# Performance work log

Hardware: AMD Instinct MI355X
Metric: run time of the kernel (lower is better)

Reference implementation:

```python
import jax, jax.numpy as jnp
import numpy as np

DIM_MODEL = 1024
NHEAD = 16
DIM_HEAD = DIM_MODEL // NHEAD


def setup_inputs() -> dict:
    key = jax.random.key(0)
    k1, k2, k3, k4 = jax.random.split(key, 4)
    x = jax.random.normal(k1, (4, 2048, DIM_MODEL), dtype=jnp.float32)
    # nn.Linear weights: PyTorch stores [out, in]; we keep [in, out] for x @ W.
    s = 1.0 / np.sqrt(DIM_MODEL)
    w_qkv = jax.random.uniform(k2, (DIM_MODEL, 3 * DIM_MODEL), jnp.float32, -s, s)
    w_out = jax.random.uniform(k3, (DIM_MODEL, DIM_MODEL), jnp.float32, -s, s)
    b_out = jax.random.uniform(k4, (DIM_MODEL,), jnp.float32, -s, s)
    return {"x": x, "w_qkv": w_qkv, "w_out": w_out, "b_out": b_out}


def reference(x, w_qkv, w_out, b_out):
    b, n, _ = x.shape
    scale = DIM_HEAD ** -0.5
    qkv = x @ w_qkv                              # [b, n, 3*dim]
    q, k, v = jnp.split(qkv, 3, axis=-1)
    def split_heads(t):                          # [b, n, h*d] -> [b, h, n, d]
        return t.reshape(b, n, NHEAD, DIM_HEAD).transpose(0, 2, 1, 3)
    q, k, v = split_heads(q), split_heads(k), split_heads(v)
    attn = jnp.einsum('bhnd,bhmd->bhnm', q, k) * scale
    attn = jax.nn.softmax(attn, axis=-1)
    out = jnp.einsum('bhnm,bhmd->bhnd', attn, v)
    out = out.transpose(0, 2, 1, 3).reshape(b, n, NHEAD * DIM_HEAD)
    return out @ w_out + b_out
```

## Files before the change

### kernel.cpp

```cpp
#include <hip/hip_runtime.h>
#include <math.h>

#define DM   1024
#define NH   16
#define DH   64
#define SEQ  2048
#define BATCH 4
#define QSCALE 0.18033688011112042f

typedef __attribute__((ext_vector_type(8)))  short short8;
typedef __attribute__((ext_vector_type(4)))  float f32x4;
typedef __attribute__((ext_vector_type(16))) float f32x16;

static __device__ __forceinline__ unsigned short f2bf(float f) {
    unsigned u = __float_as_uint(f);
    unsigned r = (u + 0x7fffu + ((u >> 16) & 1u)) >> 16;
    return (unsigned short)r;
}

#define GLD(gp, lp) __builtin_amdgcn_global_load_lds( \
    (const __attribute__((address_space(1))) void*)(gp), \
    (__attribute__((address_space(3))) void*)(lp), 16, 0, 0)

__global__ __launch_bounds__(256) void prep_all(
    const float* __restrict__ x, unsigned short* __restrict__ x_h,
    const float* __restrict__ w_qkv, unsigned short* __restrict__ wqT_h,
    const float* __restrict__ w_out, unsigned short* __restrict__ woT_h)
{
    __shared__ float t[32][33];
    const int bid = blockIdx.x;
    const int tid = threadIdx.x;
    if (bid < 8192) {
        int i = bid * 256 + tid;
        float4 v = reinterpret_cast<const float4*>(x)[i];
        ushort4 h;
        h.x = f2bf(v.x); h.y = f2bf(v.y); h.z = f2bf(v.z); h.w = f2bf(v.w);
        reinterpret_cast<ushort4*>(x_h)[i] = h;
        return;
    }
    const float* in;
    unsigned short* outT;
    int K = DM, N, n0, k0;
    if (bid < 8192 + 3072) {
        int bb = bid - 8192;
        in = w_qkv; outT = wqT_h; N = 3 * DM;
        n0 = (bb % 96) * 32; k0 = (bb / 96) * 32;
    } else {
        int bb = bid - 8192 - 3072;
        in = w_out; outT = woT_h; N = DM;
        n0 = (bb % 32) * 32; k0 = (bb / 32) * 32;
    }
    const int tx = tid & 31, ty = tid >> 5;
    #pragma unroll
    for (int r = 0; r < 32; r += 8)
        t[ty + r][tx] = in[(size_t)(k0 + ty + r) * N + n0 + tx];
    __syncthreads();
    #pragma unroll
    for (int r = 0; r < 32; r += 8)
        outT[(size_t)(n0 + ty + r) * K + k0 + tx] = f2bf(t[tx][ty + r]);
}

__global__ __launch_bounds__(256) void gemm_qkv(
    const unsigned short* __restrict__ Ah, const unsigned short* __restrict__ Bh,
    unsigned short* __restrict__ Qh, unsigned short* __restrict__ Kph,
    unsigned short* __restrict__ Vph, int M, int N, int K)
{
    __shared__ __align__(16) unsigned short sAh[128 * 32];
    __shared__ __align__(16) unsigned short sBh[128 * 32];

    const int tid = threadIdx.x;
    const int l = tid & 63, w = tid >> 6;
    const int wr = w >> 1, wc = w & 1;

    int nwg = gridDim.x * gridDim.y;
    int lin = blockIdx.x + gridDim.x * blockIdx.y;
    int cpx = nwg >> 3;
    int nl = (lin & 7) * cpx + (lin >> 3);
    const int bm = (nl % gridDim.x) * 128, bn = (nl / gridDim.x) * 128;

    const int srow = w * 32 + (l >> 2);
    const int scol = (l & 3) * 8;
    const size_t a0 = (size_t)(bm + srow) * K + scol;
    const size_t a1 = (size_t)(bm + srow + 16) * K + scol;
    const size_t b0 = (size_t)(bn + srow) * K + scol;
    const size_t b1 = (size_t)(bn + srow + 16) * K + scol;

    const int fr = l & 15;
    const int fk = (l >> 4) * 8;

    f32x4 acc[4][4];
    #pragma unroll
    for (int i = 0; i < 4; ++i)
        #pragma unroll
        for (int j = 0; j < 4; ++j)
            acc[i][j] = (f32x4){0.f, 0.f, 0.f, 0.f};

    for (int k0 = 0; k0 < K; k0 += 32) {
        __syncthreads();
        GLD(Ah + a0 + k0, sAh + w * 1024);
        GLD(Ah + a1 + k0, sAh + w * 1024 + 512);
        GLD(Bh + b0 + k0, sBh + w * 1024);
        GLD(Bh + b1 + k0, sBh + w * 1024 + 512);
        __syncthreads();

        short8 vah[4], vbh[4];
        #pragma unroll
        for (int i = 0; i < 4; ++i) {
            int ar = (wr * 64 + i * 16 + fr) * 32 + fk;
            int br = (wc * 64 + i * 16 + fr) * 32 + fk;
            vah[i] = *reinterpret_cast<const short8*>(&sAh[ar]);
            vbh[i] = *reinterpret_cast<const short8*>(&sBh[br]);
        }
        __builtin_amdgcn_s_setprio(1);
        #pragma unroll
        for (int i = 0; i < 4; ++i)
            #pragma unroll
            for (int j = 0; j < 4; ++j)
                acc[i][j] = __builtin_amdgcn_mfma_f32_16x16x32_bf16(vah[i], vbh[j], acc[i][j], 0, 0, 0);
        __builtin_amdgcn_s_setprio(0);
    }

    #pragma unroll
    for (int i = 0; i < 4; ++i) {
        #pragma unroll
        for (int j = 0; j < 4; ++j) {
            int row0 = bm + wr * 64 + i * 16 + (l >> 4) * 4;
            int col  = bn + wc * 64 + j * 16 + fr;
            if (col < 1024) {
                #pragma unroll
                for (int r = 0; r < 4; ++r)
                    Qh[(size_t)(row0 + r) * 1024 + col] = f2bf(acc[i][j][r] * QSCALE);
            } else if (col < 2048) {
                int sec = col - 1024, head = sec >> 6, d = sec & 63;
                int pK = ((d >> 4) << 1) | ((d >> 3) & 1);
                int d7 = d & 7;
                #pragma unroll
                for (int r = 0; r < 4; ++r) {
                    int row = row0 + r;
                    int bb = row >> 11, seq = row & 2047;
                    int kt = seq >> 6, k64 = seq & 63;
                    int p = ((k64 >> 5) << 3) + pK;
                    size_t addr = ((((size_t)(bb * 16 + head) * 32 + kt) * 512)
                                   + p * 32 + (k64 & 31)) * 8 + d7;
                    Kph[addr] = f2bf(acc[i][j][r]);
                }
            } else {
                int sec = col - 2048, head = sec >> 6, d = sec & 63;
                int row = row0;
                int bb = row >> 11, seq = row & 2047;
                int kt = seq >> 6, k64 = seq & 63, k16 = k64 & 15;
                int p = ((d >> 5) << 3) + ((k64 >> 4) << 1) + ((k16 >> 2) & 1);
                int jbase = (k16 >> 3) << 2;
                size_t chunk = (((size_t)(bb * 16 + head) * 32 + kt) * 512
                                + p * 32 + (d & 31));
                ushort4 v4;
                #pragma unroll
                for (int r = 0; r < 4; ++r)
                    ((unsigned short*)&v4)[r] = f2bf(acc[i][j][r]);
                *reinterpret_cast<ushort4*>(Vph + chunk * 8 + jbase) = v4;
            }
        }
    }
}

__global__ __launch_bounds__(256) void gemm_out(
    const unsigned short* __restrict__ Ah, const unsigned short* __restrict__ Bh,
    const float* __restrict__ bias, float* __restrict__ C, int M, int N, int K)
{
    __shared__ __align__(16) unsigned short sAh[128 * 32];
    __shared__ __align__(16) unsigned short sBh[128 * 32];

    const int tid = threadIdx.x;
    const int l = tid & 63, w = tid >> 6;
    const int wr = w >> 1, wc = w & 1;

    int nwg = gridDim.x * gridDim.y;
    int lin = blockIdx.x + gridDim.x * blockIdx.y;
    int cpx = nwg >> 3;
    int nl = (lin & 7) * cpx + (lin >> 3);
    const int bm = (nl % gridDim.x) * 128, bn = (nl / gridDim.x) * 128;

    const int srow = w * 32 + (l >> 2);
    const int scol = (l & 3) * 8;
    const size_t a0 = (size_t)(bm + srow) * K + scol;
    const size_t a1 = (size_t)(bm + srow + 16) * K + scol;
    const size_t b0 = (size_t)(bn + srow) * K + scol;
    const size_t b1 = (size_t)(bn + srow + 16) * K + scol;

    const int fr = l & 15;
    const int fk = (l >> 4) * 8;

    f32x4 acc[4][4];
    #pragma unroll
    for (int i = 0; i < 4; ++i)
        #pragma unroll
        for (int j = 0; j < 4; ++j)
            acc[i][j] = (f32x4){0.f, 0.f, 0.f, 0.f};

    for (int k0 = 0; k0 < K; k0 += 32) {
        __syncthreads();
        GLD(Ah + a0 + k0, sAh + w * 1024);
        GLD(Ah + a1 + k0, sAh + w * 1024 + 512);
        GLD(Bh + b0 + k0, sBh + w * 1024);
        GLD(Bh + b1 + k0, sBh + w * 1024 + 512);
        __syncthreads();

        short8 vah[4], vbh[4];
        #pragma unroll
        for (int i = 0; i < 4; ++i) {
            int ar = (wr * 64 + i * 16 + fr) * 32 + fk;
            int br = (wc * 64 + i * 16 + fr) * 32 + fk;
            vah[i] = *reinterpret_cast<const short8*>(&sAh[ar]);
            vbh[i] = *reinterpret_cast<const short8*>(&sBh[br]);
        }
        __builtin_amdgcn_s_setprio(1);
        #pragma unroll
        for (int i = 0; i < 4; ++i)
            #pragma unroll
            for (int j = 0; j < 4; ++j)
                acc[i][j] = __builtin_amdgcn_mfma_f32_16x16x32_bf16(vah[i], vbh[j], acc[i][j], 0, 0, 0);
        __builtin_amdgcn_s_setprio(0);
    }

    #pragma unroll
    for (int i = 0; i < 4; ++i) {
        #pragma unroll
        for (int j = 0; j < 4; ++j) {
            int row = bm + wr * 64 + i * 16 + (l >> 4) * 4;
            int col = bn + wc * 64 + j * 16 + fr;
            float bb = bias[col];
            #pragma unroll
            for (int r = 0; r < 4; ++r)
                C[(size_t)(row + r) * N + col] = acc[i][j][r] + bb;
        }
    }
}

__global__ __launch_bounds__(256, 3) void flash_attn_mfma(
    const unsigned short* __restrict__ Qh,
    const unsigned short* __restrict__ Kph,
    const unsigned short* __restrict__ Vph,
    unsigned short* __restrict__ out_hi)
{
    __shared__ __align__(16) unsigned short sK[2][4096];
    __shared__ __align__(16) unsigned short sV[2][4096];

    int lin = blockIdx.x + 16 * blockIdx.y + 256 * blockIdx.z;
    int nlid = (lin & 7) * 128 + (lin >> 3);
    const int qt = nlid & 15, head = (nlid >> 4) & 15, b = nlid >> 8;

    const int tid = threadIdx.x;
    const int l = tid & 63, w = tid >> 6;
    const int q5 = l & 31, hf = l >> 5;

    const int bh = b * NH + head;
    const size_t kvb = (size_t)bh * 32 * 512 * 8;

    #define STAGE_KV(cbuf, kt_) do {                                          \
        _Pragma("unroll")                                                     \
        for (int i2 = 0; i2 < 2; ++i2) {                                      \
            int ch = (w * 2 + i2) * 64 + l;                                   \
            size_t s8 = kvb + ((size_t)(kt_) * 512 + ch) * 8;                 \
            GLD(Kph + s8, (char*)&sK[cbuf][0] + ch * 16);                     \
            GLD(Vph + s8, (char*)&sV[cbuf][0] + ch * 16);                     \
        }                                                                     \
    } while (0)

    const int qrow = qt * 128 + w * 32 + q5;
    short8 qhr[4];
    {
        const size_t qb = ((size_t)b * SEQ + qrow) * 1024 + head * 64;
        #pragma unroll
        for (int s = 0; s < 4; ++s)
            qhr[s] = *reinterpret_cast<const short8*>(Qh + qb + s * 16 + hf * 8);
    }

    float l_ = 0.f;
    f32x16 oacc0, oacc1, fz;
    #pragma unroll
    for (int r = 0; r < 16; ++r) { oacc0[r] = 0.f; oacc1[r] = 0.f; fz[r] = 0.f; }

    union FragU { unsigned u[4]; short8 s8; };
    short8 pbh[4];

    STAGE_KV(0, 0);
    int cur = 0;

    for (int kt = 0; kt < SEQ / 64; ++kt) {
        __syncthreads();
        if (kt + 1 < SEQ / 64) STAGE_KV(cur ^ 1, kt + 1);

        const char* kb = (const char*)&sK[cur][0] + l * 16;

        f32x16 sacc0, sacc1;
        __builtin_amdgcn_s_setprio(1);
        {
            short8 k0h = *reinterpret_cast<const short8*>(kb);
            short8 k1h = *reinterpret_cast<const short8*>(kb + 4 * 1024);
            sacc0 = __builtin_amdgcn_mfma_f32_32x32x16_bf16(k0h, qhr[0], fz, 0, 0, 0);
            sacc1 = __builtin_amdgcn_mfma_f32_32x32x16_bf16(k1h, qhr[0], fz, 0, 0, 0);
        }
        #pragma unroll
        for (int s = 1; s < 4; ++s) {
            short8 k0h = *reinterpret_cast<const short8*>(kb + s * 1024);
            short8 k1h = *reinterpret_cast<const short8*>(kb + (4 + s) * 1024);
            sacc0 = __builtin_amdgcn_mfma_f32_32x32x16_bf16(k0h, qhr[s], sacc0, 0, 0, 0);
            sacc1 = __builtin_amdgcn_mfma_f32_32x32x16_bf16(k1h, qhr[s], sacc1, 0, 0, 0);
        }
        __builtin_amdgcn_s_setprio(0);

        float ssum = 0.f;
        #pragma unroll
        for (int jt = 0; jt < 2; ++jt) {
            float pv[16];
            #pragma unroll
            for (int r = 0; r < 16; ++r) {
                float sv = (jt == 0) ? sacc0[r] : sacc1[r];
                pv[r] = __builtin_amdgcn_exp2f(sv);
                ssum += pv[r];
            }
            FragU f0, f1;
            asm("v_cvt_pk_bf16_f32 %0, %1, %2" : "=v"(f0.u[0]) : "v"(pv[0]),  "v"(pv[1]));
            asm("v_cvt_pk_bf16_f32 %0, %1, %2" : "=v"(f0.u[1]) : "v"(pv[2]),  "v"(pv[3]));
            asm("v_cvt_pk_bf16_f32 %0, %1, %2" : "=v"(f0.u[2]) : "v"(pv[4]),  "v"(pv[5]));
            asm("v_cvt_pk_bf16_f32 %0, %1, %2" : "=v"(f0.u[3]) : "v"(pv[6]),  "v"(pv[7]));
            asm("v_cvt_pk_bf16_f32 %0, %1, %2" : "=v"(f1.u[0]) : "v"(pv[8]),  "v"(pv[9]));
            asm("v_cvt_pk_bf16_f32 %0, %1, %2" : "=v"(f1.u[1]) : "v"(pv[10]), "v"(pv[11]));
            asm("v_cvt_pk_bf16_f32 %0, %1, %2" : "=v"(f1.u[2]) : "v"(pv[12]), "v"(pv[13]));
            asm("v_cvt_pk_bf16_f32 %0, %1, %2" : "=v"(f1.u[3]) : "v"(pv[14]), "v"(pv[15]));
            pbh[jt * 2 + 0] = f0.s8;
            pbh[jt * 2 + 1] = f1.s8;
        }
        l_ += ssum;

        const char* vb = (const char*)&sV[cur][0] + l * 16;
        __builtin_amdgcn_s_setprio(1);
        #pragma unroll
        for (int kpv = 0; kpv < 4; ++kpv) {
            short8 v0h = *reinterpret_cast<const short8*>(vb + kpv * 1024);
            short8 v1h = *reinterpret_cast<const short8*>(vb + (4 + kpv) * 1024);
            oacc0 = __builtin_amdgcn_mfma_f32_32x32x16_bf16(v0h, pbh[kpv], oacc0, 0, 0, 0);
            oacc1 = __builtin_amdgcn_mfma_f32_32x32x16_bf16(v1h, pbh[kpv], oacc1, 0, 0, 0);
        }
        __builtin_amdgcn_s_setprio(0);
        cur ^= 1;
    }

    l_ += __shfl_xor(l_, 32);
    float linv = 1.f / l_;
    #pragma unroll
    for (int dt = 0; dt < 2; ++dt) {
        #pragma unroll
        for (int rq = 0; rq < 4; ++rq) {
            int dbase = dt * 32 + rq * 8 + 4 * hf;
            ushort4 h4;
            #pragma unroll
            for (int c = 0; c < 4; ++c) {
                float v = ((dt == 0) ? oacc0[rq * 4 + c] : oacc1[rq * 4 + c]) * linv;
                ((unsigned short*)&h4)[c] = f2bf(v);
            }
            size_t o = ((size_t)b * SEQ + qrow) * DM + head * 64 + dbase;
            *reinterpret_cast<ushort4*>(out_hi + o) = h4;
        }
    }
    #undef STAGE_KV
}

extern "C" void kernel_launch(void* const* d_in, const int* in_sizes, int n_in,
                              void* d_out, int out_size, void* d_ws, size_t ws_size,
                              hipStream_t stream) {
    const float* x     = (const float*)d_in[0];
    const float* w_qkv = (const float*)d_in[1];
    const float* w_out = (const float*)d_in[2];
    const float* b_out = (const float*)d_in[3];
    float* out = (float*)d_out;

    const int M = BATCH * SEQ;

    char* ws = (char*)d_ws;
    unsigned short* x_h   = (unsigned short*)ws;                         ws += (size_t)M * DM * 2;
    unsigned short* Qh    = (unsigned short*)ws;                         ws += (size_t)M * DM * 2;
    unsigned short* Kp_h  = (unsigned short*)ws;                         ws += (size_t)M * DM * 2;
    unsigned short* Vp_h  = (unsigned short*)ws;                         ws += (size_t)M * DM * 2;
    unsigned short* wqT_h = (unsigned short*)ws;                         ws += (size_t)3072 * DM * 2;
    unsigned short* woT_h = (unsigned short*)ws;                         ws += (size_t)DM * DM * 2;
    unsigned short* at_hi = (unsigned short*)ws;

    dim3 blk(256);

    prep_all<<<dim3(8192 + 3072 + 1024), blk, 0, stream>>>(
        x, x_h, w_qkv, wqT_h, w_out, woT_h);

    gemm_qkv<<<dim3(M / 128, 3 * DM / 128), blk, 0, stream>>>(
        x_h, wqT_h, Qh, Kp_h, Vp_h, M, 3 * DM, DM);

    flash_attn_mfma<<<dim3(SEQ / 128, NH, BATCH), blk, 0, stream>>>(
        Qh, Kp_h, Vp_h, at_hi);

    gemm_out<<<dim3(M / 128, DM / 128), blk, 0, stream>>>(
        at_hi, woT_h, b_out, out, M, DM, DM);
}
```

Baseline: 196.9 us.

## Pre-pack GEMM operands into MFMA fragment-tiled layout for contiguous LDS loads

The prep kernel now writes x and both weight matrices as bf16 in a tile-packed layout of 128x32 blocks, ordered so that each GEMM k-step is one contiguous 8 KB chunk. The attention kernel writes its output in the same packed layout. Both GEMMs then issue fully contiguous global-to-LDS loads and read fragments with lane-linear LDS addresses, which removes strided row access and likely LDS bank conflicts. The trade-off is that the transposing weight pack now uses strided scalar reads without an LDS transpose, and the GEMMs are hard-coded to fixed shapes.

```diff
diff --git a/kernel.cpp b/kernel.cpp
--- a/kernel.cpp
+++ b/kernel.cpp
@@ -3,7 +3,6 @@
 
 #define DM   1024
 #define NH   16
-#define DH   64
 #define SEQ  2048
 #define BATCH 4
 #define QSCALE 0.18033688011112042f
@@ -22,51 +21,52 @@
     (const __attribute__((address_space(1))) void*)(gp), \
     (__attribute__((address_space(3))) void*)(lp), 16, 0, 0)
 
-__global__ __launch_bounds__(256) void prep_all(
-    const float* __restrict__ x, unsigned short* __restrict__ x_h,
-    const float* __restrict__ w_qkv, unsigned short* __restrict__ wqT_h,
-    const float* __restrict__ w_out, unsigned short* __restrict__ woT_h)
+__global__ __launch_bounds__(256) void prep_pack(
+    const float* __restrict__ x,     unsigned short* __restrict__ xp,
+    const float* __restrict__ wq,    unsigned short* __restrict__ wqp,
+    const float* __restrict__ wo,    unsigned short* __restrict__ wop)
 {
-    __shared__ float t[32][33];
-    const int bid = blockIdx.x;
-    const int tid = threadIdx.x;
-    if (bid < 8192) {
-        int i = bid * 256 + tid;
-        float4 v = reinterpret_cast<const float4*>(x)[i];
-        ushort4 h;
-        h.x = f2bf(v.x); h.y = f2bf(v.y); h.z = f2bf(v.z); h.w = f2bf(v.w);
-        reinterpret_cast<ushort4*>(x_h)[i] = h;
-        return;
-    }
-    const float* in;
-    unsigned short* outT;
-    int K = DM, N, n0, k0;
-    if (bid < 8192 + 3072) {
-        int bb = bid - 8192;
-        in = w_qkv; outT = wqT_h; N = 3 * DM;
-        n0 = (bb % 96) * 32; k0 = (bb / 96) * 32;
-    } else {
-        int bb = bid - 8192 - 3072;
-        in = w_out; outT = woT_h; N = DM;
-        n0 = (bb % 32) * 32; k0 = (bb / 32) * 32;
-    }
-    const int tx = tid & 31, ty = tid >> 5;
-    #pragma unroll
-    for (int r = 0; r < 32; r += 8)
-        t[ty + r][tx] = in[(size_t)(k0 + ty + r) * N + n0 + tx];
-    __syncthreads();
-    #pragma unroll
-    for (int r = 0; r < 32; r += 8)
-        outT[(size_t)(n0 + ty + r) * K + k0 + tx] = f2bf(t[tx][ty + r]);
+    const int bid = blockIdx.x, t = threadIdx.x;
+    const float* src; unsigned short* dst; int C, tile_n, tile_k; bool trans;
+    if (bid < 2048)      { src = x;  dst = xp;  C = 1024; trans = false;
+                           tile_n = bid >> 5;          tile_k = bid & 31; }
+    else if (bid < 2816) { int bb = bid - 2048; src = wq; dst = wqp; C = 3072;
+                           trans = true; tile_n = bb >> 5; tile_k = bb & 31; }
+    else                 { int bb = bid - 2816; src = wo; dst = wop; C = 1024;
+                           trans = true; tile_n = bb >> 5; tile_k = bb & 31; }
+
+    union U8 { unsigned short u[8]; uint4 v; };
+    #pragma unroll
+    for (int cc = 0; cc < 2; ++cc) {
+        int c = t + cc * 256;
+        int fr = c & 15, hi = (c >> 4) & 3, i = (c >> 6) & 3, half = c >> 8;
+        int row = tile_n * 128 + half * 64 + i * 16 + fr;
+        int k0  = tile_k * 32 + hi * 8;
+        float v[8];
+        if (!trans) {
+            float4 f0 = *reinterpret_cast<const float4*>(src + (size_t)row * C + k0);
+            float4 f1 = *reinterpret_cast<const float4*>(src + (size_t)row * C + k0 + 4);
+            v[0] = f0.x; v[1] = f0.y; v[2] = f0.z; v[3] = f0.w;
+            v[4] = f1.x; v[5] = f1.y; v[6] = f1.z; v[7] = f1.w;
+        } else {
+            #pragma unroll
+            for (int j = 0; j < 8; ++j)
+                v[j] = src[(size_t)(k0 + j) * C + row];
+        }
+        U8 o;
+        #pragma unroll
+        for (int j = 0; j < 8; ++j) o.u[j] = f2bf(v[j]);
+        *reinterpret_cast<uint4*>(dst + ((size_t)(tile_n * 32 + tile_k) * 512 + c) * 8) = o.v;
+    }
 }
 
 __global__ __launch_bounds__(256) void gemm_qkv(
-    const unsigned short* __restrict__ Ah, const unsigned short* __restrict__ Bh,
+    const unsigned short* __restrict__ Ap, const unsigned short* __restrict__ Bp,
     unsigned short* __restrict__ Qh, unsigned short* __restrict__ Kph,
-    unsigned short* __restrict__ Vph, int M, int N, int K)
+    unsigned short* __restrict__ Vph)
 {
-    __shared__ __align__(16) unsigned short sAh[128 * 32];
-    __shared__ __align__(16) unsigned short sBh[128 * 32];
+    __shared__ __align__(16) unsigned short sA[4096];
+    __shared__ __align__(16) unsigned short sB[4096];
 
     const int tid = threadIdx.x;
     const int l = tid & 63, w = tid >> 6;
@@ -78,15 +78,12 @@
     int nl = (lin & 7) * cpx + (lin >> 3);
     const int bm = (nl % gridDim.x) * 128, bn = (nl / gridDim.x) * 128;
 
-    const int srow = w * 32 + (l >> 2);
-    const int scol = (l & 3) * 8;
-    const size_t a0 = (size_t)(bm + srow) * K + scol;
-    const size_t a1 = (size_t)(bm + srow + 16) * K + scol;
-    const size_t b0 = (size_t)(bn + srow) * K + scol;
-    const size_t b1 = (size_t)(bn + srow + 16) * K + scol;
+    const size_t abase = (size_t)(bm >> 7) * 32 * 4096 + (size_t)(w * 128 + l) * 8;
+    const size_t bbase = (size_t)(bn >> 7) * 32 * 4096 + (size_t)(w * 128 + l) * 8;
+    char* dA = (char*)sA + w * 2048;
+    char* dB = (char*)sB + w * 2048;
 
     const int fr = l & 15;
-    const int fk = (l >> 4) * 8;
 
     f32x4 acc[4][4];
     #pragma unroll
@@ -95,21 +92,19 @@
         for (int j = 0; j < 4; ++j)
             acc[i][j] = (f32x4){0.f, 0.f, 0.f, 0.f};
 
-    for (int k0 = 0; k0 < K; k0 += 32) {
-        __syncthreads();
-        GLD(Ah + a0 + k0, sAh + w * 1024);
-        GLD(Ah + a1 + k0, sAh + w * 1024 + 512);
-        GLD(Bh + b0 + k0, sBh + w * 1024);
-        GLD(Bh + b1 + k0, sBh + w * 1024 + 512);
+    for (int kit = 0; kit < 32; ++kit) {
+        __syncthreads();
+        GLD(Ap + abase + (size_t)kit * 4096,       dA);
+        GLD(Ap + abase + (size_t)kit * 4096 + 512, dA + 1024);
+        GLD(Bp + bbase + (size_t)kit * 4096,       dB);
+        GLD(Bp + bbase + (size_t)kit * 4096 + 512, dB + 1024);
         __syncthreads();
 
         short8 vah[4], vbh[4];
         #pragma unroll
         for (int i = 0; i < 4; ++i) {
-            int ar = (wr * 64 + i * 16 + fr) * 32 + fk;
-            int br = (wc * 64 + i * 16 + fr) * 32 + fk;
-            vah[i] = *reinterpret_cast<const short8*>(&sAh[ar]);
-            vbh[i] = *reinterpret_cast<const short8*>(&sBh[br]);
+            vah[i] = *reinterpret_cast<const short8*>((char*)sA + wr * 4096 + i * 1024 + l * 16);
+            vbh[i] = *reinterpret_cast<const short8*>((char*)sB + wc * 4096 + i * 1024 + l * 16);
         }
         __builtin_amdgcn_s_setprio(1);
         #pragma unroll
@@ -164,11 +159,11 @@
 }
 
 __global__ __launch_bounds__(256) void gemm_out(
-    const unsigned short* __restrict__ Ah, const unsigned short* __restrict__ Bh,
-    const float* __restrict__ bias, float* __restrict__ C, int M, int N, int K)
+    const unsigned short* __restrict__ Ap, const unsigned short* __restrict__ Bp,
+    const float* __restrict__ bias, float* __restrict__ C)
 {
-    __shared__ __align__(16) unsigned short sAh[128 * 32];
-    __shared__ __align__(16) unsigned short sBh[128 * 32];
+    __shared__ __align__(16) unsigned short sA[4096];
+    __shared__ __align__(16) unsigned short sB[4096];
 
     const int tid = threadIdx.x;
     const int l = tid & 63, w = tid >> 6;
@@ -180,15 +175,12 @@
     int nl = (lin & 7) * cpx + (lin >> 3);
     const int bm = (nl % gridDim.x) * 128, bn = (nl / gridDim.x) * 128;
 
-    const int srow = w * 32 + (l >> 2);
-    const int scol = (l & 3) * 8;
-    const size_t a0 = (size_t)(bm + srow) * K + scol;
-    const size_t a1 = (size_t)(bm + srow + 16) * K + scol;
-    const size_t b0 = (size_t)(bn + srow) * K + scol;
-    const size_t b1 = (size_t)(bn + srow + 16) * K + scol;
+    const size_t abase = (size_t)(bm >> 7) * 32 * 4096 + (size_t)(w * 128 + l) * 8;
+    const size_t bbase = (size_t)(bn >> 7) * 32 * 4096 + (size_t)(w * 128 + l) * 8;
+    char* dA = (char*)sA + w * 2048;
+    char* dB = (char*)sB + w * 2048;
 
     const int fr = l & 15;
-    const int fk = (l >> 4) * 8;
 
     f32x4 acc[4][4];
     #pragma unroll
@@ -197,21 +189,19 @@
         for (int j = 0; j < 4; ++j)
             acc[i][j] = (f32x4){0.f, 0.f, 0.f, 0.f};
 
-    for (int k0 = 0; k0 < K; k0 += 32) {
-        __syncthreads();
-        GLD(Ah + a0 + k0, sAh + w * 1024);
-        GLD(Ah + a1 + k0, sAh + w * 1024 + 512);
-        GLD(Bh + b0 + k0, sBh + w * 1024);
-        GLD(Bh + b1 + k0, sBh + w * 1024 + 512);
+    for (int kit = 0; kit < 32; ++kit) {
+        __syncthreads();
+        GLD(Ap + abase + (size_t)kit * 4096,       dA);
+        GLD(Ap + abase + (size_t)kit * 4096 + 512, dA + 1024);
+        GLD(Bp + bbase + (size_t)kit * 4096,       dB);
+        GLD(Bp + bbase + (size_t)kit * 4096 + 512, dB + 1024);
         __syncthreads();
 
         short8 vah[4], vbh[4];
         #pragma unroll
         for (int i = 0; i < 4; ++i) {
-            int ar = (wr * 64 + i * 16 + fr) * 32 + fk;
-            int br = (wc * 64 + i * 16 + fr) * 32 + fk;
-            vah[i] = *reinterpret_cast<const short8*>(&sAh[ar]);
-            vbh[i] = *reinterpret_cast<const short8*>(&sBh[br]);
+            vah[i] = *reinterpret_cast<const short8*>((char*)sA + wr * 4096 + i * 1024 + l * 16);
+            vbh[i] = *reinterpret_cast<const short8*>((char*)sB + wc * 4096 + i * 1024 + l * 16);
         }
         __builtin_amdgcn_s_setprio(1);
         #pragma unroll
@@ -231,7 +221,7 @@
             float bb = bias[col];
             #pragma unroll
             for (int r = 0; r < 4; ++r)
-                C[(size_t)(row + r) * N + col] = acc[i][j][r] + bb;
+                C[(size_t)(row + r) * DM + col] = acc[i][j][r] + bb;
         }
     }
 }
@@ -240,7 +230,7 @@
     const unsigned short* __restrict__ Qh,
     const unsigned short* __restrict__ Kph,
     const unsigned short* __restrict__ Vph,
-    unsigned short* __restrict__ out_hi)
+    unsigned short* __restrict__ at_p)
 {
     __shared__ __align__(16) unsigned short sK[2][4096];
     __shared__ __align__(16) unsigned short sV[2][4096];
@@ -348,19 +338,23 @@
 
     l_ += __shfl_xor(l_, 32);
     float linv = 1.f / l_;
+    const int rowin = w * 32 + q5;
+    const int half = rowin >> 6, ii = (rowin >> 4) & 3;
+    const int frr = q5 & 15;
+    const int tile_m = b * 16 + qt;
     #pragma unroll
     for (int dt = 0; dt < 2; ++dt) {
+        size_t tbase = ((size_t)(tile_m * 32) + head * 2 + dt) * 512;
         #pragma unroll
         for (int rq = 0; rq < 4; ++rq) {
-            int dbase = dt * 32 + rq * 8 + 4 * hf;
             ushort4 h4;
             #pragma unroll
             for (int c = 0; c < 4; ++c) {
                 float v = ((dt == 0) ? oacc0[rq * 4 + c] : oacc1[rq * 4 + c]) * linv;
                 ((unsigned short*)&h4)[c] = f2bf(v);
             }
-            size_t o = ((size_t)b * SEQ + qrow) * DM + head * 64 + dbase;
-            *reinterpret_cast<ushort4*>(out_hi + o) = h4;
+            int ch = half * 256 + ii * 64 + rq * 16 + frr;
+            *reinterpret_cast<ushort4*>(at_p + (tbase + ch) * 8 + 4 * hf) = h4;
         }
     }
     #undef STAGE_KV
@@ -378,25 +372,25 @@
     const int M = BATCH * SEQ;
 
     char* ws = (char*)d_ws;
-    unsigned short* x_h   = (unsigned short*)ws;                         ws += (size_t)M * DM * 2;
+    unsigned short* x_p   = (unsigned short*)ws;                         ws += (size_t)M * DM * 2;
     unsigned short* Qh    = (unsigned short*)ws;                         ws += (size_t)M * DM * 2;
     unsigned short* Kp_h  = (unsigned short*)ws;                         ws += (size_t)M * DM * 2;
     unsigned short* Vp_h  = (unsigned short*)ws;                         ws += (size_t)M * DM * 2;
-    unsigned short* wqT_h = (unsigned short*)ws;                         ws += (size_t)3072 * DM * 2;
-    unsigned short* woT_h = (unsigned short*)ws;                         ws += (size_t)DM * DM * 2;
-    unsigned short* at_hi = (unsigned short*)ws;
+    unsigned short* wq_p  = (unsigned short*)ws;                         ws += (size_t)3072 * DM * 2;
+    unsigned short* wo_p  = (unsigned short*)ws;                         ws += (size_t)DM * DM * 2;
+    unsigned short* at_p  = (unsigned short*)ws;
 
     dim3 blk(256);
 
-    prep_all<<<dim3(8192 + 3072 + 1024), blk, 0, stream>>>(
-        x, x_h, w_qkv, wqT_h, w_out, woT_h);
+    prep_pack<<<dim3(2048 + 768 + 256), blk, 0, stream>>>(
+        x, x_p, w_qkv, wq_p, w_out, wo_p);
 
     gemm_qkv<<<dim3(M / 128, 3 * DM / 128), blk, 0, stream>>>(
-        x_h, wqT_h, Qh, Kp_h, Vp_h, M, 3 * DM, DM);
+        x_p, wq_p, Qh, Kp_h, Vp_h);
 
     flash_attn_mfma<<<dim3(SEQ / 128, NH, BATCH), blk, 0, stream>>>(
-        Qh, Kp_h, Vp_h, at_hi);
+        Qh, Kp_h, Vp_h, at_p);
 
     gemm_out<<<dim3(M / 128, DM / 128), blk, 0, stream>>>(
-        at_hi, woT_h, b_out, out, M, DM, DM);
-}
+        at_p, wo_p, b_out, out);
+}
```

Result: slower. 203.1 us (+3.1%).
